# Performance work log

Hardware: AMD Instinct MI355X
Metric: run time of the kernel (lower is better)

Reference implementation:

```python
import jax, jax.numpy as jnp
import numpy as np

K = 32
TEMPERATURE = 0.1
RTOL, ATOL = 1e-5, 1e-5


def _embed(x, W1, b1, W2, b2, W3, b3):
    h = jax.nn.gelu(x @ W1.T + b1, approximate=False)
    h = jax.nn.gelu(h @ W2.T + b2, approximate=False)
    return jax.nn.sigmoid(h @ W3.T + b3)


def setup_inputs() -> dict:
    key = jax.random.key(0)
    ks = jax.random.split(key, 9)
    Q, N, D_IN, D_E = 256, 16384, 256, 64
    s = lambda fan_in: 1.0 / np.sqrt(fan_in)
    return {
        "x": jax.random.normal(ks[0], (Q, D_IN), jnp.float32),
        "support_x": jax.random.normal(ks[1], (N, D_IN), jnp.float32),
        "support_labels": jax.random.uniform(ks[2], (N, 1), jnp.float32),
        "W1": jax.random.normal(ks[3], (D_E, D_IN), jnp.float32) * s(D_IN),
        "b1": jax.random.normal(ks[4], (D_E,), jnp.float32) * s(D_IN),
        "W2": jax.random.normal(ks[5], (D_E, D_E), jnp.float32) * s(D_E),
        "b2": jax.random.normal(ks[6], (D_E,), jnp.float32) * s(D_E),
        "W3": jax.random.normal(ks[7], (D_E, D_E), jnp.float32) * s(D_E),
        "b3": jax.random.normal(ks[8], (D_E,), jnp.float32) * s(D_E),
    }


def reference(x, support_x, support_labels, W1, b1, W2, b2, W3, b3):
    # query embeddings [Q, D]; support embeddings [N, D] (set_support is no_grad)
    q = _embed(x, W1, b1, W2, b2, W3, b3)
    s = jax.lax.stop_gradient(_embed(support_x, W1, b1, W2, b2, W3, b3))
    # torch.cdist p=2 via expanded squared distances
    d2 = (jnp.sum(q * q, -1)[:, None] + jnp.sum(s * s, -1)[None, :]
          - 2.0 * (q @ s.T))
    dist = jnp.sqrt(jnp.maximum(d2, 0.0))  # [Q, N]
    # isclose mask: |q - s| <= atol + rtol*|s|, all over feature dim
    close = jnp.abs(q[:, None, :] - s[None, :, :]) <= (ATOL + RTOL * jnp.abs(s)[None, :, :])
    mask = jnp.all(close, axis=-1)  # [Q, N]
    dist = jnp.where(mask, jnp.inf, dist)
    # top-k smallest distances
    neg_top, idx = jax.lax.top_k(-dist, K)  # [Q, K]
    topd = -neg_top
    neighbor_labels = support_labels[idx].squeeze(-1)  # [Q, K]
    weights = jax.nn.softmax(-topd / TEMPERATURE, axis=1)
    return jnp.sum(weights * neighbor_labels, axis=1)  # [Q]
```

## Files before the change

### kernel.cpp

```cpp
#include <hip/hip_runtime.h>
#include <math.h>

#define D_IN   256
#define D_E    64
#define N_SUP  16384
#define NQ     256
#define KSEL   32
#define RTOLC  1e-5f
#define ATOLC  1e-5f
#define INV_T  10.0f

#define CHUNK  512
#define NCH    32
#define QG     16
#define NQG    16

typedef unsigned long long ull;

__device__ __forceinline__ float gelu_exact(float x) {
    return 0.5f * x * (1.0f + erff(x * 0.70710678118654752440f));
}

__global__ __launch_bounds__(256) void prep_w(
    const float* __restrict__ W1, const float* __restrict__ W2,
    const float* __restrict__ W3,
    float* __restrict__ W1T, float* __restrict__ W2T, float* __restrict__ W3T)
{
    const int t = blockIdx.x * 256 + threadIdx.x;
    const int stride = gridDim.x * 256;
    for (int o = t; o < D_E * D_IN; o += stride) {
        int f = o >> 8, k = o & 255;
        W1T[k * D_E + f] = W1[o];
    }
    for (int o = t; o < D_E * D_E; o += stride) {
        int f = o >> 6, k = o & 63;
        W2T[k * D_E + f] = W2[o];
        W3T[k * D_E + f] = W3[o];
    }
}

__global__ __launch_bounds__(256) void embed_kernel(
    const float* __restrict__ sx, const float* __restrict__ x,
    const float* __restrict__ W1T, const float* __restrict__ b1,
    const float* __restrict__ W2T, const float* __restrict__ b2,
    const float* __restrict__ W3T, const float* __restrict__ b3,
    float* __restrict__ s_emb, float* __restrict__ s_norm,
    float* __restrict__ q_emb, float* __restrict__ q_norm)
{
    __shared__ float hx[32][68];
    __shared__ float nsq[32][17];

    const int tid = threadIdx.x;
    const int rp  = tid >> 4;
    const int fg  = tid & 15;
    const bool isq = blockIdx.x >= (N_SUP / 32);
    const int rowb = (isq ? (int)blockIdx.x - N_SUP / 32 : (int)blockIdx.x) * 32;
    const float* src = (isq ? x : sx) + (size_t)rowb * D_IN;
    const float4* X4  = reinterpret_cast<const float4*>(src);
    const float4* W14 = reinterpret_cast<const float4*>(W1T);
    const float4* W24 = reinterpret_cast<const float4*>(W2T);
    const float4* W34 = reinterpret_cast<const float4*>(W3T);
    const int r0 = 2 * rp, r1 = 2 * rp + 1;

    #define FMA4(acc_, w_, xs_)                                                \
        acc_.x = fmaf(w_.x, xs_, acc_.x); acc_.y = fmaf(w_.y, xs_, acc_.y);    \
        acc_.z = fmaf(w_.z, xs_, acc_.z); acc_.w = fmaf(w_.w, xs_, acc_.w);

    float4 acc0 = reinterpret_cast<const float4*>(b1)[fg];
    float4 acc1 = acc0;
    #pragma unroll 4
    for (int k4 = 0; k4 < 64; ++k4) {
        float4 xa = X4[r0 * 64 + k4];
        float4 xb = X4[r1 * 64 + k4];
        float4 wa = W14[(4 * k4 + 0) * 16 + fg];
        float4 wb = W14[(4 * k4 + 1) * 16 + fg];
        float4 wc = W14[(4 * k4 + 2) * 16 + fg];
        float4 wd = W14[(4 * k4 + 3) * 16 + fg];
        FMA4(acc0, wa, xa.x); FMA4(acc0, wb, xa.y);
        FMA4(acc0, wc, xa.z); FMA4(acc0, wd, xa.w);
        FMA4(acc1, wa, xb.x); FMA4(acc1, wb, xb.y);
        FMA4(acc1, wc, xb.z); FMA4(acc1, wd, xb.w);
    }
    *reinterpret_cast<float4*>(&hx[r0][fg * 4]) = make_float4(
        gelu_exact(acc0.x), gelu_exact(acc0.y), gelu_exact(acc0.z), gelu_exact(acc0.w));
    *reinterpret_cast<float4*>(&hx[r1][fg * 4]) = make_float4(
        gelu_exact(acc1.x), gelu_exact(acc1.y), gelu_exact(acc1.z), gelu_exact(acc1.w));

    float4 c0 = reinterpret_cast<const float4*>(b2)[fg];
    float4 c1 = c0;
    #pragma unroll 4
    for (int k4 = 0; k4 < 16; ++k4) {
        float4 xa = *reinterpret_cast<const float4*>(&hx[r0][k4 * 4]);
        float4 xb = *reinterpret_cast<const float4*>(&hx[r1][k4 * 4]);
        float4 wa = W24[(4 * k4 + 0) * 16 + fg];
        float4 wb = W24[(4 * k4 + 1) * 16 + fg];
        float4 wc = W24[(4 * k4 + 2) * 16 + fg];
        float4 wd = W24[(4 * k4 + 3) * 16 + fg];
        FMA4(c0, wa, xa.x); FMA4(c0, wb, xa.y);
        FMA4(c0, wc, xa.z); FMA4(c0, wd, xa.w);
        FMA4(c1, wa, xb.x); FMA4(c1, wb, xb.y);
        FMA4(c1, wc, xb.z); FMA4(c1, wd, xb.w);
    }
    *reinterpret_cast<float4*>(&hx[r0][fg * 4]) = make_float4(
        gelu_exact(c0.x), gelu_exact(c0.y), gelu_exact(c0.z), gelu_exact(c0.w));
    *reinterpret_cast<float4*>(&hx[r1][fg * 4]) = make_float4(
        gelu_exact(c1.x), gelu_exact(c1.y), gelu_exact(c1.z), gelu_exact(c1.w));

    float4 d0 = reinterpret_cast<const float4*>(b3)[fg];
    float4 d1 = d0;
    #pragma unroll 4
    for (int k4 = 0; k4 < 16; ++k4) {
        float4 xa = *reinterpret_cast<const float4*>(&hx[r0][k4 * 4]);
        float4 xb = *reinterpret_cast<const float4*>(&hx[r1][k4 * 4]);
        float4 wa = W34[(4 * k4 + 0) * 16 + fg];
        float4 wb = W34[(4 * k4 + 1) * 16 + fg];
        float4 wc = W34[(4 * k4 + 2) * 16 + fg];
        float4 wd = W34[(4 * k4 + 3) * 16 + fg];
        FMA4(d0, wa, xa.x); FMA4(d0, wb, xa.y);
        FMA4(d0, wc, xa.z); FMA4(d0, wd, xa.w);
        FMA4(d1, wa, xb.x); FMA4(d1, wb, xb.y);
        FMA4(d1, wc, xb.z); FMA4(d1, wd, xb.w);
    }
    #undef FMA4

    float* E   = isq ? q_emb  : s_emb;
    float* Nrm = isq ? q_norm : s_norm;
    {
        float e0 = 1.0f / (1.0f + expf(-d0.x));
        float e1 = 1.0f / (1.0f + expf(-d0.y));
        float e2 = 1.0f / (1.0f + expf(-d0.z));
        float e3 = 1.0f / (1.0f + expf(-d0.w));
        *reinterpret_cast<float4*>(E + (size_t)(rowb + r0) * D_E + fg * 4) =
            make_float4(e0, e1, e2, e3);
        nsq[r0][fg] = fmaf(e0, e0, fmaf(e1, e1, fmaf(e2, e2, e3 * e3)));
    }
    {
        float e0 = 1.0f / (1.0f + expf(-d1.x));
        float e1 = 1.0f / (1.0f + expf(-d1.y));
        float e2 = 1.0f / (1.0f + expf(-d1.z));
        float e3 = 1.0f / (1.0f + expf(-d1.w));
        *reinterpret_cast<float4*>(E + (size_t)(rowb + r1) * D_E + fg * 4) =
            make_float4(e0, e1, e2, e3);
        nsq[r1][fg] = fmaf(e0, e0, fmaf(e1, e1, fmaf(e2, e2, e3 * e3)));
    }
    __syncthreads();
    if (tid < 32) {
        float s = 0.0f;
        #pragma unroll
        for (int g = 0; g < 16; ++g) s += nsq[tid][g];
        Nrm[rowb + tid] = s;
    }
}

__global__ __launch_bounds__(512, 2) void knn_phaseA(
    const float* __restrict__ s_emb, const float* __restrict__ s_norm,
    const float* __restrict__ q_emb, const float* __restrict__ q_norm,
    const float* __restrict__ labels, ull* __restrict__ cand)
{
    __shared__ float tile[2][64 * 68];
    __shared__ ull   win_l[QG][KSEL];

    const int tid  = threadIdx.x;
    const int lane = tid & 63;
    const int wid  = tid >> 6;
    const int qg   = blockIdx.x >> 5;
    const int sc   = blockIdx.x & 31;
    const int qiu  = __builtin_amdgcn_readfirstlane(qg * QG + 2 * wid);
    const float* q0 = q_emb + (size_t)qiu * D_E;
    const float* q1 = q0 + D_E;
    const float  qn0 = q_norm[qiu];
    const float  qn1 = q_norm[qiu + 1];

    #pragma unroll
    for (int i = 0; i < 2; ++i) {
        int g = i * 512 + tid;
        int row = g >> 4, c4 = g & 15;
        float4 v = *reinterpret_cast<const float4*>(
            s_emb + (size_t)(sc * CHUNK + row) * D_E + c4 * 4);
        *reinterpret_cast<float4*>(&tile[0][row * 68 + c4 * 4]) = v;
    }
    __syncthreads();

    float d2a[8], d2b[8];
    #pragma unroll
    for (int s = 0; s < 8; ++s) {
        const int b = s & 1;
        float4 p0, p1;
        if (s < 7) {
            p0 = *reinterpret_cast<const float4*>(
                s_emb + (size_t)(sc * CHUNK + (s + 1) * 64 + (tid >> 4)) * D_E + (tid & 15) * 4);
            p1 = *reinterpret_cast<const float4*>(
                s_emb + (size_t)(sc * CHUNK + (s + 1) * 64 + ((512 + tid) >> 4)) * D_E + (tid & 15) * 4);
        }
        const float* tr = &tile[b][lane * 68];
        float a0 = 0.0f, a1 = 0.0f;
        #pragma unroll
        for (int c = 0; c < 16; ++c) {
            float4 sv = *reinterpret_cast<const float4*>(tr + c * 4);
            a0 = fmaf(q0[c * 4 + 0], sv.x, a0);
            a0 = fmaf(q0[c * 4 + 1], sv.y, a0);
            a0 = fmaf(q0[c * 4 + 2], sv.z, a0);
            a0 = fmaf(q0[c * 4 + 3], sv.w, a0);
            a1 = fmaf(q1[c * 4 + 0], sv.x, a1);
            a1 = fmaf(q1[c * 4 + 1], sv.y, a1);
            a1 = fmaf(q1[c * 4 + 2], sv.z, a1);
            a1 = fmaf(q1[c * 4 + 3], sv.w, a1);
        }
        const int grow = sc * CHUNK + s * 64 + lane;
        const float sn = s_norm[grow];
        float d20 = fmaxf(qn0 + sn - 2.0f * a0, 0.0f);
        float d21 = fmaxf(qn1 + sn - 2.0f * a1, 0.0f);
        if (d20 < 1e-3f) {
            bool close = true;
            for (int k = 0; k < D_E; ++k) {
                float svk = tr[k];
                close = close && (fabsf(q0[k] - svk) <= (ATOLC + RTOLC * fabsf(svk)));
            }
            if (close) d20 = INFINITY;
        }
        if (d21 < 1e-3f) {
            bool close = true;
            for (int k = 0; k < D_E; ++k) {
                float svk = tr[k];
                close = close && (fabsf(q1[k] - svk) <= (ATOLC + RTOLC * fabsf(svk)));
            }
            if (close) d21 = INFINITY;
        }
        d2a[s] = d20;
        d2b[s] = d21;
        if (s < 7) {
            *reinterpret_cast<float4*>(&tile[b ^ 1][(tid >> 4) * 68 + (tid & 15) * 4]) = p0;
            *reinterpret_cast<float4*>(&tile[b ^ 1][((512 + tid) >> 4) * 68 + (tid & 15) * 4]) = p1;
        }
        __syncthreads();
    }

    const int h  = lane >> 5;
    const unsigned l5 = lane & 31;
    ull sk[16];
    #pragma unroll
    for (int j = 0; j < 8; ++j) {
        float ta  = __shfl_xor(d2a[j], 32);
        float tbx = __shfl_xor(d2b[j], 32);
        float vlo = h ? tbx : d2a[j];
        float vhi = h ? d2b[j] : ta;
        unsigned rlo = (unsigned)(j * 64) + l5;
        sk[j]     = ((ull)__float_as_uint(vlo) << 9) | rlo;
        sk[j + 8] = ((ull)__float_as_uint(vhi) << 9) | (rlo + 32);
    }

    #pragma unroll
    for (int k = 2; k <= 16; k <<= 1) {
        #pragma unroll
        for (int j = k >> 1; j > 0; j >>= 1) {
            #pragma unroll
            for (int i = 0; i < 16; ++i) {
                int ixj = i ^ j;
                if (ixj > i) {
                    ull a_ = sk[i], b_ = sk[ixj];
                    bool up = (i & k) == 0;
                    bool c_ = up ? (b_ < a_) : (a_ < b_);
                    sk[i] = c_ ? b_ : a_; sk[ixj] = c_ ? a_ : b_;
                }
            }
        }
    }

    ull lkey = sk[0];
    for (int it = 0; it < KSEL; ++it) {
        unsigned lv = (unsigned)(lkey >> 9);
        unsigned m = lv;
        #pragma unroll
        for (int off = 1; off < 32; off <<= 1) {
            unsigned o = __shfl_xor(m, off);
            m = o < m ? o : m;
        }
        ull tb = __ballot(lv == m);
        bool cond;
        if (__popcll(tb) != 2) {
            unsigned rr = (lv == m) ? (unsigned)(lkey & 511u) : 0xffffffffu;
            unsigned rm = rr;
            #pragma unroll
            for (int off = 1; off < 32; off <<= 1) {
                unsigned o = __shfl_xor(rm, off);
                rm = o < rm ? o : rm;
            }
            cond = (lv == m) && ((unsigned)(lkey & 511u) == rm);
        } else {
            cond = (lv == m);
        }
        if (cond) {
            win_l[2 * wid + h][it] = lkey;
            #pragma unroll
            for (int j = 0; j < 15; ++j) sk[j] = sk[j + 1];
            sk[15] = ~0ull;
            lkey = sk[0];
        }
    }

    {
        const int e = (int)l5;
        ull m = win_l[2 * wid + h][e];
        unsigned gidx = (unsigned)(sc * CHUNK) + (unsigned)(m & 511u);
        float lab = labels[gidx];
        ull* dst = cand + ((size_t)(qg * QG + 2 * wid + h) * NCH + sc) * KSEL;
        dst[e] = ((ull)(unsigned)(m >> 9) << 32) | (ull)__float_as_uint(lab);
    }
}

__global__ __launch_bounds__(256) void knn_phaseB(
    const ull* __restrict__ cand, float* __restrict__ out)
{
    const int lane = threadIdx.x & 63;
    const int wid  = threadIdx.x >> 6;
    const int q    = blockIdx.x * 4 + wid;

    const bool act = lane < NCH;
    const ull* lst = cand + ((size_t)q * NCH + (lane & 31)) * KSEL;
    int ptr = 0;
    ull cur = act ? lst[0] : ~0ull;

    float d0 = 0.0f, sw = 0.0f, sl = 0.0f;
    for (int it = 0; it < KSEL; ++it) {
        unsigned mv = (unsigned)(cur >> 32);
        unsigned ml = (unsigned)cur;
        #pragma unroll
        for (int off = 1; off < 32; off <<= 1) {
            unsigned ov = __shfl_xor(mv, off);
            unsigned ol = __shfl_xor(ml, off);
            bool take = (ov < mv) || (ov == mv && (lane & off));
            mv = take ? ov : mv;
            ml = take ? ol : ml;
        }
        ull bl = __ballot(act && (unsigned)(cur >> 32) == mv);
        int wl = (int)(__ffsll((long long)bl) - 1);
        if (lane == wl) {
            ++ptr;
            cur = (ptr < KSEL) ? lst[ptr] : ~0ull;
        }
        if (lane == 0) {
            float d = sqrtf(__uint_as_float(mv));
            if (it == 0) d0 = d;
            float w = expf((d0 - d) * INV_T);
            sw += w;
            sl += w * __uint_as_float(ml);
        }
    }
    if (lane == 0) out[q] = sl / sw;
}

extern "C" void kernel_launch(void* const* d_in, const int* in_sizes, int n_in,
                              void* d_out, int out_size, void* d_ws, size_t ws_size,
                              hipStream_t stream) {
    const float* x      = (const float*)d_in[0];
    const float* sx     = (const float*)d_in[1];
    const float* labels = (const float*)d_in[2];
    const float* W1     = (const float*)d_in[3];
    const float* b1     = (const float*)d_in[4];
    const float* W2     = (const float*)d_in[5];
    const float* b2     = (const float*)d_in[6];
    const float* W3     = (const float*)d_in[7];
    const float* b3     = (const float*)d_in[8];
    float* out = (float*)d_out;

    float* ws     = (float*)d_ws;
    float* s_emb  = ws;
    float* s_norm = s_emb + (size_t)N_SUP * D_E;
    float* q_emb  = s_norm + N_SUP;
    float* q_norm = q_emb + (size_t)NQ * D_E;
    ull*   cand   = (ull*)(q_norm + NQ);
    float* W1T    = (float*)(cand + (size_t)NQ * NCH * KSEL);
    float* W2T    = W1T + D_IN * D_E;
    float* W3T    = W2T + D_E * D_E;

    prep_w<<<32, 256, 0, stream>>>(W1, W2, W3, W1T, W2T, W3T);
    embed_kernel<<<(N_SUP + NQ) / 32, 256, 0, stream>>>(
        sx, x, W1T, b1, W2T, b2, W3T, b3, s_emb, s_norm, q_emb, q_norm);
    knn_phaseA<<<NQG * NCH, 512, 0, stream>>>(s_emb, s_norm, q_emb, q_norm,
                                              labels, cand);
    knn_phaseB<<<NQ / 4, 256, 0, stream>>>(cand, out);
}
```

Measured before the change: 109.5 us.

## Read support rows directly from global memory instead of LDS double-buffer

Removes the shared-memory double-buffered tile of support embeddings in the kNN distance kernel. Each lane now loads its support row straight from global memory, and the per-stage barriers are gone. The min-blocks launch bound is also relaxed. This cuts LDS traffic and synchronisation, but every wave re-reads the same rows with a strided, uncoalesced access pattern and relies on the caches.

```diff
diff --git a/kernel.cpp b/kernel.cpp
--- a/kernel.cpp
+++ b/kernel.cpp
@@ -152,13 +152,12 @@
     }
 }
 
-__global__ __launch_bounds__(512, 2) void knn_phaseA(
+__global__ __launch_bounds__(512) void knn_phaseA(
     const float* __restrict__ s_emb, const float* __restrict__ s_norm,
     const float* __restrict__ q_emb, const float* __restrict__ q_norm,
     const float* __restrict__ labels, ull* __restrict__ cand)
 {
-    __shared__ float tile[2][64 * 68];
-    __shared__ ull   win_l[QG][KSEL];
+    __shared__ ull win_l[QG][KSEL];
 
     const int tid  = threadIdx.x;
     const int lane = tid & 63;
@@ -171,32 +170,15 @@
     const float  qn0 = q_norm[qiu];
     const float  qn1 = q_norm[qiu + 1];
 
-    #pragma unroll
-    for (int i = 0; i < 2; ++i) {
-        int g = i * 512 + tid;
-        int row = g >> 4, c4 = g & 15;
-        float4 v = *reinterpret_cast<const float4*>(
-            s_emb + (size_t)(sc * CHUNK + row) * D_E + c4 * 4);
-        *reinterpret_cast<float4*>(&tile[0][row * 68 + c4 * 4]) = v;
-    }
-    __syncthreads();
-
     float d2a[8], d2b[8];
     #pragma unroll
     for (int s = 0; s < 8; ++s) {
-        const int b = s & 1;
-        float4 p0, p1;
-        if (s < 7) {
-            p0 = *reinterpret_cast<const float4*>(
-                s_emb + (size_t)(sc * CHUNK + (s + 1) * 64 + (tid >> 4)) * D_E + (tid & 15) * 4);
-            p1 = *reinterpret_cast<const float4*>(
-                s_emb + (size_t)(sc * CHUNK + (s + 1) * 64 + ((512 + tid) >> 4)) * D_E + (tid & 15) * 4);
-        }
-        const float* tr = &tile[b][lane * 68];
+        const int grow = sc * CHUNK + s * 64 + lane;
+        const float* rp = s_emb + (size_t)grow * D_E;
         float a0 = 0.0f, a1 = 0.0f;
         #pragma unroll
         for (int c = 0; c < 16; ++c) {
-            float4 sv = *reinterpret_cast<const float4*>(tr + c * 4);
+            float4 sv = *reinterpret_cast<const float4*>(rp + c * 4);
             a0 = fmaf(q0[c * 4 + 0], sv.x, a0);
             a0 = fmaf(q0[c * 4 + 1], sv.y, a0);
             a0 = fmaf(q0[c * 4 + 2], sv.z, a0);
@@ -206,14 +188,13 @@
             a1 = fmaf(q1[c * 4 + 2], sv.z, a1);
             a1 = fmaf(q1[c * 4 + 3], sv.w, a1);
         }
-        const int grow = sc * CHUNK + s * 64 + lane;
         const float sn = s_norm[grow];
         float d20 = fmaxf(qn0 + sn - 2.0f * a0, 0.0f);
         float d21 = fmaxf(qn1 + sn - 2.0f * a1, 0.0f);
         if (d20 < 1e-3f) {
             bool close = true;
             for (int k = 0; k < D_E; ++k) {
-                float svk = tr[k];
+                float svk = rp[k];
                 close = close && (fabsf(q0[k] - svk) <= (ATOLC + RTOLC * fabsf(svk)));
             }
             if (close) d20 = INFINITY;
@@ -221,18 +202,13 @@
         if (d21 < 1e-3f) {
             bool close = true;
             for (int k = 0; k < D_E; ++k) {
-                float svk = tr[k];
+                float svk = rp[k];
                 close = close && (fabsf(q1[k] - svk) <= (ATOLC + RTOLC * fabsf(svk)));
             }
             if (close) d21 = INFINITY;
         }
         d2a[s] = d20;
         d2b[s] = d21;
-        if (s < 7) {
-            *reinterpret_cast<float4*>(&tile[b ^ 1][(tid >> 4) * 68 + (tid & 15) * 4]) = p0;
-            *reinterpret_cast<float4*>(&tile[b ^ 1][((512 + tid) >> 4) * 68 + (tid & 15) * 4]) = p1;
-        }
-        __syncthreads();
     }
 
     const int h  = lane >> 5;
```

Measured after the change: 139.6 us. 27.5% more time.
